# Kernel tuning notes

Measured on AMD Instinct MI355X. Metric: run time of the kernel, lower is better.

Reference implementation:

```python
import jax, jax.numpy as jnp
import numpy as np

TEMPERATURE = 0.7
TOP_K = 50
TOP_P = 0.9
B, S, H, V = 2, 1024, 512, 50257


def setup_inputs() -> dict:
    key = jax.random.key(0)
    k1, k2 = jax.random.split(key)
    x = jax.random.normal(k1, (B, S, H), dtype=jnp.float32)
    # small init scale keeps logits in a realistic range so nucleus mass is spread
    W = jax.random.normal(k2, (V, H), dtype=jnp.float32) * 0.02
    b = jnp.zeros((V,), dtype=jnp.float32)
    return {"x": x, "W": W, "b": b}


def _top_k_top_p_filtering(logits):
    # --- top-k: mask everything below the k-th largest value ---
    top_k_vals = jax.lax.top_k(logits, TOP_K)[0]          # [B,S,K]
    min_top_k = top_k_vals[..., -1:]                       # [B,S,1]
    logits = jnp.where(logits < min_top_k, -jnp.inf, logits)
    # --- top-p (nucleus): sort descending, cumsum of probs, drop tail ---
    sorted_idx = jnp.argsort(-logits, axis=-1)             # descending order
    sorted_logits = jnp.take_along_axis(logits, sorted_idx, axis=-1)
    cum_probs = jnp.cumsum(jax.nn.softmax(sorted_logits, axis=-1), axis=-1)
    sorted_logits = jnp.where(cum_probs > TOP_P, -jnp.inf, sorted_logits)
    # NOTE: the original torch code does gather(sorted_logits, index=sorted_indices)
    # (forward-gather, not inverse scatter). We replicate that exact math.
    logits = jnp.take_along_axis(sorted_logits, sorted_idx, axis=-1)
    return logits


def reference(x, W, b):
    # ExampleModel: single linear projection to vocab logits [B,S,V]
    logits = jnp.einsum('bsh,vh->bsv', x, W) + b
    logits = logits / TEMPERATURE
    filtered = _top_k_top_p_filtering(logits)
    return jax.nn.softmax(filtered, axis=-1)
```

## Files before the change

kernel.cpp:

```cpp
#include <hip/hip_runtime.h>
#include <math.h>

#define TEMP 0.7f
#define TOPK 50
#define TOPP 0.9f
#define M_TOT 2048
#define K_DIM 512
#define V_DIM 50257
#define NPAD 50304
#define KP 1536
#define BM 256
#define BN 128
#define BKE 64
#define NSTEP (KP / BKE)
#define NBN (NPAD / BN)
#define NBM (M_TOT / BM)

typedef short s16x8 __attribute__((ext_vector_type(8)));
typedef float f32x4 __attribute__((ext_vector_type(4)));

#define MFMA_16x16x32_BF16(acc, va, vb) \
  asm("v_mfma_f32_16x16x32_bf16 %0, %1, %2, %0" : "+v"(acc) : "v"(va), "v"(vb))

__device__ __forceinline__ unsigned short bf16_rn(float x) {
  unsigned u = __float_as_uint(x);
  unsigned r = u + 0x7FFFu + ((u >> 16) & 1u);
  return (unsigned short)(r >> 16);
}
__device__ __forceinline__ float bf16_to_f(unsigned short h) {
  return __uint_as_float(((unsigned)h) << 16);
}
__device__ __forceinline__ unsigned f2key(float f) {
  unsigned u = __float_as_uint(f);
  return (u & 0x80000000u) ? ~u : (u | 0x80000000u);
}

#define NQX (M_TOT * (K_DIM / 4))
#define NQW (NPAD * (K_DIM / 4))

__global__ __launch_bounds__(256) void conv_kernel(const float* __restrict__ X,
                                                   const float* __restrict__ W,
                                                   unsigned short* __restrict__ Xp,
                                                   unsigned short* __restrict__ Wp) {
  int idx = blockIdx.x * 256 + threadIdx.x;
  float4 v;
  unsigned short* dst;
  size_t base;
  int mode;
  if (idx < NQX) {
    int row = idx >> 7, q = idx & 127;
    v = reinterpret_cast<const float4*>(X)[idx];
    dst = Xp;
    base = (size_t)row * KP + q * 4;
    mode = 0;
  } else {
    int wi = idx - NQX;
    if (wi >= NQW) return;
    int row = wi >> 7, q = wi & 127;
    v = make_float4(0.f, 0.f, 0.f, 0.f);
    if (row < V_DIM) v = reinterpret_cast<const float4*>(W)[(size_t)row * 128 + q];
    dst = Wp;
    base = (size_t)row * KP + q * 4;
    mode = 1;
  }
  float vv[4] = {v.x, v.y, v.z, v.w};
  unsigned short hi[4], lo[4];
#pragma unroll
  for (int j = 0; j < 4; ++j) {
    hi[j] = bf16_rn(vv[j]);
    lo[j] = bf16_rn(vv[j] - bf16_to_f(hi[j]));
  }
  ushort4 h4 = make_ushort4(hi[0], hi[1], hi[2], hi[3]);
  ushort4 l4 = make_ushort4(lo[0], lo[1], lo[2], lo[3]);
  *reinterpret_cast<ushort4*>(dst + base) = h4;
  if (mode == 0) {
    *reinterpret_cast<ushort4*>(dst + base + K_DIM) = h4;
    *reinterpret_cast<ushort4*>(dst + base + 2 * K_DIM) = l4;
  } else {
    *reinterpret_cast<ushort4*>(dst + base + K_DIM) = l4;
    *reinterpret_cast<ushort4*>(dst + base + 2 * K_DIM) = h4;
  }
}

#define SW 68

__global__ __launch_bounds__(512) void mfma_gemm_kernel(
    const unsigned short* __restrict__ Ap, const unsigned short* __restrict__ Bp,
    const float* __restrict__ Bv, float* __restrict__ C,
    unsigned* __restrict__ Tmax) {
  __shared__ __align__(16) unsigned char lds[49152];
  const int tid = threadIdx.x;
  const int w = tid >> 6, lane = tid & 63;
  const int bm = blockIdx.x * BM;
  const int bni = blockIdx.y;
  const int bn = bni * BN;
  const int wr = w >> 1, wc = w & 1;

  f32x4 acc[4][4] = {};

  for (int step = 0; step < NSTEP; ++step) {
    const int k0 = step * BKE;
#pragma unroll
    for (int l = 0; l < 4; ++l) {
      int pp = ((l * 512 + tid) << 4);
      int row = pp >> 7;
      int cb = (pp & 127) ^ ((row & 7) << 4);
      const unsigned short* ga = Ap + (size_t)(bm + row) * KP + k0 + (cb >> 1);
      __builtin_amdgcn_global_load_lds(
          (const __attribute__((address_space(1))) unsigned int*)ga,
          (__attribute__((address_space(3))) unsigned int*)(lds + pp), 16, 0, 0);
    }
#pragma unroll
    for (int l = 0; l < 2; ++l) {
      int pp = ((l * 512 + tid) << 4);
      int row = pp >> 7;
      int cb = (pp & 127) ^ ((row & 7) << 4);
      const unsigned short* gb = Bp + (size_t)(bn + row) * KP + k0 + (cb >> 1);
      __builtin_amdgcn_global_load_lds(
          (const __attribute__((address_space(1))) unsigned int*)gb,
          (__attribute__((address_space(3))) unsigned int*)(lds + 32768 + pp), 16, 0, 0);
    }
    __syncthreads();
#pragma unroll
    for (int kk = 0; kk < 2; ++kk) {
      const int kbyte = kk * 64 + ((lane >> 4) << 4);
      s16x8 a[4], b[4];
#pragma unroll
      for (int i = 0; i < 4; ++i) {
        int row = (wr << 6) + (i << 4) + (lane & 15);
        int byte = (row << 7) + (kbyte ^ ((row & 7) << 4));
        a[i] = *reinterpret_cast<const s16x8*>(lds + byte);
      }
#pragma unroll
      for (int j = 0; j < 4; ++j) {
        int row = (wc << 6) + (j << 4) + (lane & 15);
        int byte = (row << 7) + (kbyte ^ ((row & 7) << 4));
        b[j] = *reinterpret_cast<const s16x8*>(lds + 32768 + byte);
      }
#pragma unroll
      for (int i = 0; i < 4; ++i)
#pragma unroll
        for (int j = 0; j < 4; ++j) MFMA_16x16x32_BF16(acc[i][j], a[i], b[j]);
    }
    __syncthreads();
  }

  __syncthreads();
  float* wreg = reinterpret_cast<float*>(lds) + w * (16 * SW);
  float mx[4][4];
#pragma unroll
  for (int i = 0; i < 4; ++i)
#pragma unroll
    for (int r = 0; r < 4; ++r) mx[i][r] = -INFINITY;

#pragma unroll
  for (int i = 0; i < 4; ++i) {
#pragma unroll
    for (int j = 0; j < 4; ++j) {
      int n = bn + (wc << 6) + (j << 4) + (lane & 15);
      float bv = (n < V_DIM) ? Bv[n] : 0.f;
#pragma unroll
      for (int r = 0; r < 4; ++r) {
        float val = (acc[i][j][r] + bv) / TEMP;
        wreg[(((lane >> 4) << 2) + r) * SW + (j << 4) + (lane & 15)] = val;
        if (n < V_DIM) mx[i][r] = fmaxf(mx[i][r], val);
      }
    }
    int row = lane >> 2;
    int m = bm + (wr << 6) + (i << 4) + row;
#pragma unroll
    for (int it = 0; it < 4; ++it) {
      int c = ((lane & 3) << 2) + (it << 4);
      f32x4 v4 = *reinterpret_cast<const f32x4*>(wreg + row * SW + c);
      int n4 = bn + (wc << 6) + c;
      if (n4 + 3 < V_DIM) {
        *reinterpret_cast<f32x4*>(&C[(size_t)m * V_DIM + n4]) = v4;
      } else {
#pragma unroll
        for (int e = 0; e < 4; ++e)
          if (n4 + e < V_DIM) C[(size_t)m * V_DIM + n4 + e] = v4[e];
      }
    }
  }

  __syncthreads();
  unsigned* umax = reinterpret_cast<unsigned*>(lds);
  if (tid < BM) umax[tid] = 0;
  __syncthreads();
#pragma unroll
  for (int i = 0; i < 4; ++i) {
#pragma unroll
    for (int r = 0; r < 4; ++r) {
      float v = mx[i][r];
      v = fmaxf(v, __shfl_xor(v, 1));
      v = fmaxf(v, __shfl_xor(v, 2));
      v = fmaxf(v, __shfl_xor(v, 4));
      v = fmaxf(v, __shfl_xor(v, 8));
      if ((lane & 15) == 0)
        atomicMax(&umax[(wr << 6) + (i << 4) + ((lane >> 4) << 2) + r], f2key(v));
    }
  }
  __syncthreads();
  if (tid < BM) Tmax[(size_t)(bm + tid) * NBN + bni] = umax[tid];
}

#define CAP 1024
#define SCAP 256

__global__ __launch_bounds__(256) void select_kernel(float* __restrict__ C,
                                                     const unsigned* __restrict__ Tmax) {
  const int row = blockIdx.x;
  float* rowp = C + (size_t)row * V_DIM;
  const int tid = threadIdx.x;

  __shared__ unsigned tk[NBN];
  __shared__ short ctile[NBN];
  __shared__ unsigned s_t50;
  __shared__ float cval[CAP];
  __shared__ int cidx[CAP];
  __shared__ float sval[SCAP];
  __shared__ int sidx[SCAP];
  __shared__ float pvals[SCAP];
  __shared__ int s_cnt, s_ntile, s_nsurv, s_kc;
  __shared__ float s_invZ;

  for (int i = tid; i < NBN; i += 256) tk[i] = Tmax[(size_t)row * NBN + i];
  if (tid == 0) { s_cnt = 0; s_ntile = 0; s_nsurv = 0; }
  __syncthreads();
  for (int i = tid; i < NBN; i += 256) {
    unsigned ki = tk[i];
    int r = 0;
    for (int j = 0; j < NBN; ++j) {
      unsigned kj = tk[j];
      r += (kj > ki) || (kj == ki && j < i);
    }
    if (r == TOPK - 1) s_t50 = ki;
  }
  __syncthreads();
  const unsigned t50 = s_t50;

  for (int i = tid; i < NBN; i += 256) {
    if (tk[i] >= t50) {
      int p = atomicAdd(&s_ntile, 1);
      ctile[p] = (short)i;
    }
  }
  __syncthreads();
  const int ntile = s_ntile;

  for (int e = tid; e < ntile * BN; e += 256) {
    int ti = ctile[e >> 7];
    int n = ti * BN + (e & 127);
    if (n < V_DIM) {
      float l = rowp[n];
      if (f2key(l) >= t50) {
        int p = atomicAdd(&s_cnt, 1);
        if (p < CAP) { cval[p] = l; cidx[p] = n; }
      }
    }
  }
  __syncthreads();
  const int n = min(s_cnt, CAP);

  {
    const f32x4 z4 = {0.f, 0.f, 0.f, 0.f};
    const int NQ = V_DIM >> 2;
    f32x4* rp4 = reinterpret_cast<f32x4*>(rowp);
    for (int q = tid; q < NQ; q += 256) rp4[q] = z4;
    if (tid == 0) rowp[V_DIM - 1] = 0.f;
  }

  for (int i = tid; i < n; i += 256) {
    float vi = cval[i];
    int xi = cidx[i];
    int r = 0;
    for (int j = 0; j < n; ++j) {
      float vj = cval[j];
      if (vj > vi || (vj == vi && cidx[j] < xi)) ++r;
    }
    if (r < SCAP) { sval[r] = vi; sidx[r] = xi; }
  }
  __syncthreads();

  const float t = sval[TOPK - 1];
  for (int i = tid; i < n; i += 256)
    if (cval[i] >= t) atomicAdd(&s_nsurv, 1);
  __syncthreads();
  const int nsurv = min(s_nsurv, SCAP);

  const float m = sval[0];
  for (int i = tid; i < nsurv; i += 256) pvals[i] = expf(sval[i] - m);
  __syncthreads();
  if (tid == 0) {
    float Z0 = 0.f;
    for (int i = 0; i < nsurv; ++i) Z0 += pvals[i];
    float cum = 0.f;
    int kc = 0;
    float Z2 = 0.f;
    for (int i = 0; i < nsurv; ++i) {
      cum += pvals[i] / Z0;
      if (cum > TOPP) break;
      kc = i + 1;
      Z2 += pvals[i];
    }
    s_kc = kc;
    s_invZ = (kc > 0) ? (1.f / Z2) : 0.f;
  }
  __syncthreads();
  const int kc = s_kc;
  const float invZ = s_invZ;

  for (int q = tid; q < kc; q += 256) {
    int r = -1, less = 0;
    for (int s = 0; s < nsurv; ++s) {
      if (sidx[s] == q) r = s;
      if (sidx[s] < q) ++less;
    }
    int rank = (r >= 0) ? r : (nsurv + q - less);
    rowp[rank] = pvals[q] * invZ;
  }
}

extern "C" void kernel_launch(void* const* d_in, const int* in_sizes, int n_in,
                              void* d_out, int out_size, void* d_ws, size_t ws_size,
                              hipStream_t stream) {
  const float* X = (const float*)d_in[0];
  const float* W = (const float*)d_in[1];
  const float* Bv = (const float*)d_in[2];
  float* C = (float*)d_out;

  unsigned short* Xp = (unsigned short*)d_ws;
  unsigned short* Wp = Xp + (size_t)M_TOT * KP;
  unsigned* Tmax = (unsigned*)(Wp + (size_t)NPAD * KP);

  conv_kernel<<<(NQX + NQW + 255) / 256, 256, 0, stream>>>(X, W, Xp, Wp);
  dim3 g(NBM, NBN);
  mfma_gemm_kernel<<<g, 512, 0, stream>>>(Xp, Wp, Bv, C, Tmax);
  select_kernel<<<M_TOT, 256, 0, stream>>>(C, Tmax);
}
```

Baseline: 654.4 us.

## Write logits to workspace and zero output in conv kernel to decouple select

When the workspace is large enough, the GEMM writes logits into a separate workspace buffer, and the output is zeroed by extra threads appended to the conversion kernel. The select kernel then reads from the workspace and only scatters the surviving probabilities, with no per-row zeroing pass after its reads. This moves the full-output zero fill out of the latency-bound per-row select kernel into a bandwidth-friendly bulk pass, but total memory traffic does not shrink and needs about 400 MB of extra workspace. If the workspace is too small, it falls back to the old in-place path.

```diff
diff --git a/kernel.cpp b/kernel.cpp
--- a/kernel.cpp
+++ b/kernel.cpp
@@ -37,12 +37,22 @@
 
 #define NQX (M_TOT * (K_DIM / 4))
 #define NQW (NPAD * (K_DIM / 4))
+#define NZQ ((M_TOT * V_DIM) / 4)
 
 __global__ __launch_bounds__(256) void conv_kernel(const float* __restrict__ X,
                                                    const float* __restrict__ W,
                                                    unsigned short* __restrict__ Xp,
-                                                   unsigned short* __restrict__ Wp) {
+                                                   unsigned short* __restrict__ Wp,
+                                                   float* __restrict__ Z, int nzq) {
   int idx = blockIdx.x * 256 + threadIdx.x;
+  if (idx >= NQX + NQW) {
+    int zi = idx - (NQX + NQW);
+    if (zi < nzq) {
+      const f32x4 z4 = {0.f, 0.f, 0.f, 0.f};
+      reinterpret_cast<f32x4*>(Z)[zi] = z4;
+    }
+    return;
+  }
   float4 v;
   unsigned short* dst;
   size_t base;
@@ -55,7 +65,6 @@
     mode = 0;
   } else {
     int wi = idx - NQX;
-    if (wi >= NQW) return;
     int row = wi >> 7, q = wi & 127;
     v = make_float4(0.f, 0.f, 0.f, 0.f);
     if (row < V_DIM) v = reinterpret_cast<const float4*>(W)[(size_t)row * 128 + q];
@@ -170,9 +179,9 @@
     int m = bm + (wr << 6) + (i << 4) + row;
 #pragma unroll
     for (int it = 0; it < 4; ++it) {
-      int c = ((lane & 3) << 2) + (it << 4);
-      f32x4 v4 = *reinterpret_cast<const f32x4*>(wreg + row * SW + c);
-      int n4 = bn + (wc << 6) + c;
+      int c2 = ((lane & 3) << 2) + (it << 4);
+      f32x4 v4 = *reinterpret_cast<const f32x4*>(wreg + row * SW + c2);
+      int n4 = bn + (wc << 6) + c2;
       if (n4 + 3 < V_DIM) {
         *reinterpret_cast<f32x4*>(&C[(size_t)m * V_DIM + n4]) = v4;
       } else {
@@ -207,10 +216,13 @@
 #define CAP 1024
 #define SCAP 256
 
-__global__ __launch_bounds__(256) void select_kernel(float* __restrict__ C,
-                                                     const unsigned* __restrict__ Tmax) {
+__global__ __launch_bounds__(256) void select_kernel(const float* __restrict__ Lg,
+                                                     float* __restrict__ C,
+                                                     const unsigned* __restrict__ Tmax,
+                                                     int do_zero) {
   const int row = blockIdx.x;
-  float* rowp = C + (size_t)row * V_DIM;
+  const float* rowin = Lg + (size_t)row * V_DIM;
+  float* rowout = C + (size_t)row * V_DIM;
   const int tid = threadIdx.x;
 
   __shared__ unsigned tk[NBN];
@@ -252,7 +264,7 @@
     int ti = ctile[e >> 7];
     int n = ti * BN + (e & 127);
     if (n < V_DIM) {
-      float l = rowp[n];
+      float l = rowin[n];
       if (f2key(l) >= t50) {
         int p = atomicAdd(&s_cnt, 1);
         if (p < CAP) { cval[p] = l; cidx[p] = n; }
@@ -262,12 +274,12 @@
   __syncthreads();
   const int n = min(s_cnt, CAP);
 
-  {
+  if (do_zero) {
     const f32x4 z4 = {0.f, 0.f, 0.f, 0.f};
     const int NQ = V_DIM >> 2;
-    f32x4* rp4 = reinterpret_cast<f32x4*>(rowp);
+    f32x4* rp4 = reinterpret_cast<f32x4*>(rowout);
     for (int q = tid; q < NQ; q += 256) rp4[q] = z4;
-    if (tid == 0) rowp[V_DIM - 1] = 0.f;
+    if (tid == 0) rowout[V_DIM - 1] = 0.f;
   }
 
   for (int i = tid; i < n; i += 256) {
@@ -317,7 +329,7 @@
       if (sidx[s] < q) ++less;
     }
     int rank = (r >= 0) ? r : (nsurv + q - less);
-    rowp[rank] = pvals[q] * invZ;
+    rowout[rank] = pvals[q] * invZ;
   }
 }
 
@@ -332,9 +344,16 @@
   unsigned short* Xp = (unsigned short*)d_ws;
   unsigned short* Wp = Xp + (size_t)M_TOT * KP;
   unsigned* Tmax = (unsigned*)(Wp + (size_t)NPAD * KP);
-
-  conv_kernel<<<(NQX + NQW + 255) / 256, 256, 0, stream>>>(X, W, Xp, Wp);
+  float* Lws = (float*)(Tmax + (size_t)M_TOT * NBN);
+
+  const size_t need_big = (size_t)((char*)(Lws + (size_t)M_TOT * V_DIM) - (char*)d_ws);
+  const int big = (ws_size >= need_big);
+
+  float* Lg = big ? Lws : C;
+  const int nzq = big ? NZQ : 0;
+
+  conv_kernel<<<(NQX + NQW + nzq + 255) / 256, 256, 0, stream>>>(X, W, Xp, Wp, C, nzq);
   dim3 g(NBM, NBN);
-  mfma_gemm_kernel<<<g, 512, 0, stream>>>(Xp, Wp, Bv, C, Tmax);
-  select_kernel<<<M_TOT, 256, 0, stream>>>(C, Tmax);
-}
+  mfma_gemm_kernel<<<g, 512, 0, stream>>>(Xp, Wp, Bv, Lg, Tmax);
+  select_kernel<<<M_TOT, 256, 0, stream>>>(Lg, C, Tmax, big ? 0 : 1);
+}
```

Result: faster. 638.2 us (-2.5%).
